# Optimization experiments

Hardware: AMD Instinct MI355X
Metric: run time of the kernel (lower is better)

The kernel has to match this reference:

```python
import jax, jax.numpy as jnp
import numpy as np

DENSITY_FACTOR = 1.0
WHITE_BACKGROUND = False
FAR_DELTA = 1e4
EPS_DIST = 1e-5
EPS_ALPHA = 1e-8

N_RAYS = 65536
N_SAMPLES = 192
C_RGB = 3


def setup_inputs() -> dict:
    key = jax.random.key(0)
    k1, k2 = jax.random.split(key)
    rgba = jax.random.normal(k1, (N_RAYS, N_SAMPLES, C_RGB + 1), dtype=jnp.float32)
    # distances along each ray, sorted ascending (realistic sample depths in [0, 4))
    distance = jnp.sort(4.0 * jax.random.uniform(k2, (N_RAYS, N_SAMPLES), dtype=jnp.float32), axis=-1)
    return {"rgba": rgba, "distance": distance}


def reference(rgba, distance):
    # over_opacity_extra from hyperreel TensorReduce
    rgb = jax.nn.sigmoid(rgba[..., :-1])          # [N, S, C]
    density = rgba[..., -1]                        # [N, S]
    density = jnp.where(distance < EPS_DIST, jnp.zeros_like(density), density)
    density = jax.nn.relu(density) * DENSITY_FACTOR
    # deltas between consecutive samples; last delta is "infinite" (1e4)
    deltas = jnp.concatenate(
        [jnp.abs(distance[:, 1:] - distance[:, :-1]),
         FAR_DELTA * jnp.ones_like(distance[:, :1])], axis=1)
    alpha = 1.0 - jnp.exp(-deltas * density)       # [N, S]
    # over_composite_one: transmittance via exclusive cumprod of (1 - alpha)
    alphas_shifted = jnp.concatenate(
        [jnp.ones_like(alpha[:, :1]), 1.0 - alpha + EPS_ALPHA], axis=-1)
    trans = jnp.cumprod(alphas_shifted, axis=-1)[:, :-1]   # [N, S]
    weights = alpha * trans                                 # [N, S]
    rgb_final = jnp.einsum('ns,nsc->nc', weights, rgb)      # [N, C]
    if WHITE_BACKGROUND:
        accum = weights.sum(-1)
        rgb_final = rgb_final + (1.0 - accum[..., None])
    return rgb_final
```

## Files before the change

kernel.cpp:

```cpp
#include <hip/hip_runtime.h>
#include <math.h>

#define N_RAYS    65536
#define N_SAMPLES 192
#define FAR_DELTA 1e4f
#define EPS_DIST  1e-5f
#define EPS_ALPHA 1e-8f

__global__ __launch_bounds__(256) void composite_kernel(
    const float* __restrict__ rgba,
    const float* __restrict__ dist,
    float* __restrict__ out)
{
    const int lane = threadIdx.x & 63;
    const int ray  = blockIdx.x * 4 + (threadIdx.x >> 6);
    if (ray >= N_RAYS) return;

    const float4* __restrict__ rgba4 = (const float4*)rgba + (size_t)ray * N_SAMPLES;
    const float*  __restrict__ d     = dist + (size_t)ray * N_SAMPLES;

    float T = 1.0f;
    float r_acc = 0.f, g_acc = 0.f, b_acc = 0.f;

    #pragma unroll
    for (int c = 0; c < 3; ++c) {
        const int s = c * 64 + lane;
        float4 v = rgba4[s];
        float d0 = d[s];
        float delta = (s + 1 < N_SAMPLES) ? fabsf(d[s + 1] - d0) : FAR_DELTA;

        float density = v.w;
        density = (d0 < EPS_DIST) ? 0.0f : density;
        density = fmaxf(density, 0.0f);

        float alpha = 1.0f - __expf(-delta * density);
        float p = 1.0f - alpha + EPS_ALPHA;

        float P = p;
        #pragma unroll
        for (int off = 1; off < 64; off <<= 1) {
            float t = __shfl_up(P, off, 64);
            if (lane >= off) P *= t;
        }
        float E = __shfl_up(P, 1, 64);
        if (lane == 0) E = 1.0f;

        float w = alpha * (T * E);

        float rr = 1.0f / (1.0f + __expf(-v.x));
        float gg = 1.0f / (1.0f + __expf(-v.y));
        float bb = 1.0f / (1.0f + __expf(-v.z));

        r_acc = fmaf(w, rr, r_acc);
        g_acc = fmaf(w, gg, g_acc);
        b_acc = fmaf(w, bb, b_acc);

        T *= __shfl(P, 63, 64);
    }

    #pragma unroll
    for (int off = 32; off > 0; off >>= 1) {
        r_acc += __shfl_down(r_acc, off, 64);
        g_acc += __shfl_down(g_acc, off, 64);
        b_acc += __shfl_down(b_acc, off, 64);
    }

    if (lane == 0) {
        out[(size_t)ray * 3 + 0] = r_acc;
        out[(size_t)ray * 3 + 1] = g_acc;
        out[(size_t)ray * 3 + 2] = b_acc;
    }
}

extern "C" void kernel_launch(void* const* d_in, const int* in_sizes, int n_in,
                              void* d_out, int out_size, void* d_ws, size_t ws_size,
                              hipStream_t stream) {
    const float* rgba = (const float*)d_in[0];
    const float* dist = (const float*)d_in[1];
    float* out = (float*)d_out;

    const int rays_per_block = 4;
    dim3 grid(N_RAYS / rays_per_block);
    dim3 block(256);
    composite_kernel<<<grid, block, 0, stream>>>(rgba, dist, out);
}
```

Baseline: 300.3 us.

## Assign contiguous samples per lane and run a single wavefront scan

Each lane now handles three consecutive samples instead of three strided chunks. It forms the local product of the three transmittances and runs one 64-lane shuffle scan instead of three, then derives per-sample weights from the exclusive prefix. Loads use the nontemporal builtin, sigmoid uses a hardware reciprocal, and the neighbour distance comes from a shuffle. Each lane's memory access is now contiguous, but across lanes it is strided by 48 bytes, which changes how well global loads coalesce. The rcp approximation is slightly less precise than a full division.

```diff
diff --git a/kernel.cpp b/kernel.cpp
--- a/kernel.cpp
+++ b/kernel.cpp
@@ -7,6 +7,8 @@
 #define EPS_DIST  1e-5f
 #define EPS_ALPHA 1e-8f
 
+typedef float floatx4 __attribute__((ext_vector_type(4)));
+
 __global__ __launch_bounds__(256) void composite_kernel(
     const float* __restrict__ rgba,
     const float* __restrict__ dist,
@@ -14,49 +16,61 @@
 {
     const int lane = threadIdx.x & 63;
     const int ray  = blockIdx.x * 4 + (threadIdx.x >> 6);
-    if (ray >= N_RAYS) return;
 
-    const float4* __restrict__ rgba4 = (const float4*)rgba + (size_t)ray * N_SAMPLES;
-    const float*  __restrict__ d     = dist + (size_t)ray * N_SAMPLES;
+    const floatx4* __restrict__ rgba4 =
+        (const floatx4*)rgba + (size_t)ray * N_SAMPLES + lane * 3;
+    const float* __restrict__ d =
+        dist + (size_t)ray * N_SAMPLES + lane * 3;
 
-    float T = 1.0f;
-    float r_acc = 0.f, g_acc = 0.f, b_acc = 0.f;
+    floatx4 v0 = __builtin_nontemporal_load(rgba4 + 0);
+    floatx4 v1 = __builtin_nontemporal_load(rgba4 + 1);
+    floatx4 v2 = __builtin_nontemporal_load(rgba4 + 2);
+    float d0 = __builtin_nontemporal_load(d + 0);
+    float d1 = __builtin_nontemporal_load(d + 1);
+    float d2 = __builtin_nontemporal_load(d + 2);
+    float d3 = __shfl_down(d0, 1, 64);
 
+    float dl0 = fabsf(d1 - d0);
+    float dl1 = fabsf(d2 - d1);
+    float dl2 = (lane == 63) ? FAR_DELTA : fabsf(d3 - d2);
+
+    float den0 = (d0 < EPS_DIST) ? 0.0f : fmaxf(v0.w, 0.0f);
+    float den1 = (d1 < EPS_DIST) ? 0.0f : fmaxf(v1.w, 0.0f);
+    float den2 = (d2 < EPS_DIST) ? 0.0f : fmaxf(v2.w, 0.0f);
+
+    float t0 = __expf(-dl0 * den0);
+    float t1 = __expf(-dl1 * den1);
+    float t2 = __expf(-dl2 * den2);
+
+    float a0 = 1.0f - t0, a1 = 1.0f - t1, a2 = 1.0f - t2;
+    float p0 = t0 + EPS_ALPHA, p1 = t1 + EPS_ALPHA, p2 = t2 + EPS_ALPHA;
+
+    float e1 = p0;
+    float e2 = p0 * p1;
+    float Ltot = e2 * p2;
+
+    float P = Ltot;
     #pragma unroll
-    for (int c = 0; c < 3; ++c) {
-        const int s = c * 64 + lane;
-        float4 v = rgba4[s];
-        float d0 = d[s];
-        float delta = (s + 1 < N_SAMPLES) ? fabsf(d[s + 1] - d0) : FAR_DELTA;
+    for (int off = 1; off < 64; off <<= 1) {
+        float t = __shfl_up(P, off, 64);
+        if (lane >= off) P *= t;
+    }
+    float E = __shfl_up(P, 1, 64);
+    if (lane == 0) E = 1.0f;
 
-        float density = v.w;
-        density = (d0 < EPS_DIST) ? 0.0f : density;
-        density = fmaxf(density, 0.0f);
+    float w0 = a0 * E;
+    float w1 = a1 * E * e1;
+    float w2 = a2 * E * e2;
 
-        float alpha = 1.0f - __expf(-delta * density);
-        float p = 1.0f - alpha + EPS_ALPHA;
-
-        float P = p;
-        #pragma unroll
-        for (int off = 1; off < 64; off <<= 1) {
-            float t = __shfl_up(P, off, 64);
-            if (lane >= off) P *= t;
-        }
-        float E = __shfl_up(P, 1, 64);
-        if (lane == 0) E = 1.0f;
-
-        float w = alpha * (T * E);
-
-        float rr = 1.0f / (1.0f + __expf(-v.x));
-        float gg = 1.0f / (1.0f + __expf(-v.y));
-        float bb = 1.0f / (1.0f + __expf(-v.z));
-
-        r_acc = fmaf(w, rr, r_acc);
-        g_acc = fmaf(w, gg, g_acc);
-        b_acc = fmaf(w, bb, b_acc);
-
-        T *= __shfl(P, 63, 64);
-    }
+    float r_acc = w0 * __builtin_amdgcn_rcpf(1.0f + __expf(-v0.x))
+                + w1 * __builtin_amdgcn_rcpf(1.0f + __expf(-v1.x))
+                + w2 * __builtin_amdgcn_rcpf(1.0f + __expf(-v2.x));
+    float g_acc = w0 * __builtin_amdgcn_rcpf(1.0f + __expf(-v0.y))
+                + w1 * __builtin_amdgcn_rcpf(1.0f + __expf(-v1.y))
+                + w2 * __builtin_amdgcn_rcpf(1.0f + __expf(-v2.y));
+    float b_acc = w0 * __builtin_amdgcn_rcpf(1.0f + __expf(-v0.z))
+                + w1 * __builtin_amdgcn_rcpf(1.0f + __expf(-v1.z))
+                + w2 * __builtin_amdgcn_rcpf(1.0f + __expf(-v2.z));
 
     #pragma unroll
     for (int off = 32; off > 0; off >>= 1) {
@@ -79,8 +93,7 @@
     const float* dist = (const float*)d_in[1];
     float* out = (float*)d_out;
 
-    const int rays_per_block = 4;
-    dim3 grid(N_RAYS / rays_per_block);
+    dim3 grid(N_RAYS / 4);
     dim3 block(256);
     composite_kernel<<<grid, block, 0, stream>>>(rgba, dist, out);
 }
```

Result: faster. 289.7 us (-3.5%).
